# Optimization experiments

Measured on AMD Instinct MI355X. Metric: run time of the kernel, lower is better.

Reference implementation:

```python
import jax, jax.numpy as jnp
import numpy as np

P_DROP = 0.2
NEG_SLOPE = 0.2


def setup_inputs() -> dict:
    key = jax.random.key(0)
    ks = jax.random.split(key, 12)
    N, E = 50000, 800000
    IN, H1, H2, OUT = 256, 256, 128, 64
    x = jax.random.normal(ks[0], (N, IN), dtype=jnp.float32)
    adj_rows = jax.random.randint(ks[1], (E,), 0, N, dtype=jnp.int32)
    adj_cols = jax.random.randint(ks[2], (E,), 0, N, dtype=jnp.int32)
    adj_vals = jax.random.uniform(ks[3], (E,), dtype=jnp.float32)
    W1 = jax.random.normal(ks[4], (H1, IN), dtype=jnp.float32) * (1.0 / np.sqrt(IN))
    b1 = jax.random.normal(ks[5], (H1,), dtype=jnp.float32) * 0.01
    W2 = jax.random.normal(ks[6], (H2, H1), dtype=jnp.float32) * (1.0 / np.sqrt(H1))
    b2 = jax.random.normal(ks[7], (H2,), dtype=jnp.float32) * 0.01
    W3 = jax.random.normal(ks[8], (OUT, H2), dtype=jnp.float32) * (1.0 / np.sqrt(H2))
    b3 = jax.random.normal(ks[9], (OUT,), dtype=jnp.float32) * 0.01
    mask1 = jax.random.bernoulli(ks[10], 1.0 - P_DROP, (N, H1))
    mask2 = jax.random.bernoulli(ks[11], 1.0 - P_DROP, (N, H2))
    return {"x": x, "adj_rows": adj_rows, "adj_cols": adj_cols, "adj_vals": adj_vals,
            "W1": W1, "b1": b1, "W2": W2, "b2": b2, "W3": W3, "b3": b3,
            "mask1": mask1, "mask2": mask2}


def _spmm(rows, cols, vals, h, n_nodes):
    # sparse adjacency matmul: out[r] = sum_e vals[e] * h[cols[e]] for rows[e]==r
    msgs = vals[:, None] * h[cols]  # [E, d] irregular gather
    return jax.ops.segment_sum(msgs, rows, num_segments=n_nodes)


def _gcn_layer(x, W, b, rows, cols, vals, n_nodes):
    h = x @ W.T + b  # nn.Linear
    return _spmm(rows, cols, vals, h, n_nodes)


def reference(x, adj_rows, adj_cols, adj_vals, W1, b1, W2, b2, W3, b3, mask1, mask2):
    N = x.shape[0]
    keep = 1.0 / (1.0 - P_DROP)
    h = _gcn_layer(x, W1, b1, adj_rows, adj_cols, adj_vals, N)
    h = jnp.where(h >= 0, h, NEG_SLOPE * h)
    h = jnp.where(mask1, h * keep, 0.0)
    h = _gcn_layer(h, W2, b2, adj_rows, adj_cols, adj_vals, N)
    h = jnp.where(h >= 0, h, NEG_SLOPE * h)
    h = jnp.where(mask2, h * keep, 0.0)
    z = _gcn_layer(h, W3, b3, adj_rows, adj_cols, adj_vals, N)
    return z
```

## Files before the change

### kernel.cpp

```cpp
#include <hip/hip_runtime.h>


typedef unsigned short ushort_t;
typedef __attribute__((ext_vector_type(8))) short bf16x8;
typedef __attribute__((ext_vector_type(4))) float f32x4;
typedef __attribute__((ext_vector_type(2))) unsigned int u32x2;
typedef __attribute__((ext_vector_type(4))) unsigned int u32x4;

__device__ __forceinline__ float bf2f(ushort_t u) {
  return __uint_as_float(((unsigned int)u) << 16);
}
__device__ __forceinline__ ushort_t f2bf(float f) {
  unsigned int u = __float_as_uint(f);
  return (ushort_t)((u + 0x7FFFu + ((u >> 16) & 1u)) >> 16);
}
__device__ __forceinline__ float read_f(const void* p, int fm, size_t i) {
  return fm ? bf2f(((const ushort_t*)p)[i]) : ((const float*)p)[i];
}

__device__ __forceinline__ size_t frag_off(int m, int k, int K) {
  return (size_t)(m >> 4) * 16 * K + ((size_t)(k >> 5) << 9) +
         (((k >> 3) & 3) << 7) + ((m & 15) << 3) + (k & 7);
}

__global__ void prep_kernel(const void* __restrict__ x,
                            const void* __restrict__ m1,
                            const void* __restrict__ m2,
                            int* __restrict__ modes,
                            int* __restrict__ zero_region, int zn,
                            const void* __restrict__ W1, const void* __restrict__ W2,
                            const void* __restrict__ W3,
                            const void* __restrict__ b1, const void* __restrict__ b2,
                            const void* __restrict__ b3,
                            ushort_t* __restrict__ whi, ushort_t* __restrict__ wlo,
                            float* __restrict__ biasf,
                            int n1, int n2, int n3, int h1, int h2, int h3,
                            int K1, int K2, int K3) {
  if (blockIdx.x == 0) {
    __shared__ int bfok;
    if (threadIdx.x == 0) bfok = 1;
    __syncthreads();
    for (int i = threadIdx.x; i < 8192; i += blockDim.x) {
      ushort_t h = ((const ushort_t*)x)[i];
      int e = (h >> 7) & 0xFF;
      if (!(h == 0 || (e >= 95 && e <= 133))) atomicAnd(&bfok, 0);
    }
    __syncthreads();
    if (threadIdx.x == 0) modes[0] = bfok;
  } else if (blockIdx.x <= 2) {
    const void* p = (blockIdx.x == 1) ? m1 : m2;
    __shared__ int ok[4];
    if (threadIdx.x < 4) ok[threadIdx.x] = 1;
    __syncthreads();
    for (int i = threadIdx.x; i < 4096; i += blockDim.x) {
      unsigned int w = ((const unsigned int*)p)[i];
      if (!(w == 0u || w == 1u)) atomicAnd(&ok[0], 0);
      if (!(w == 0u || w == 0x3F800000u)) atomicAnd(&ok[1], 0);
      unsigned int h16 = w >> 16, l16 = w & 0xFFFFu;
      if (!((h16 == 0u || h16 == 0x3F80u) && (l16 == 0u || l16 == 0x3F80u)))
        atomicAnd(&ok[2], 0);
      if (((w | (w >> 8) | (w >> 16) | (w >> 24)) & 0xFEu) != 0u) atomicAnd(&ok[3], 0);
    }
    __syncthreads();
    if (threadIdx.x == 0)
      modes[blockIdx.x] = ok[0] ? 1 : (ok[1] ? 2 : (ok[2] ? 3 : 0));
  } else if (blockIdx.x < 35) {
    __shared__ int bfok;
    if (threadIdx.x == 0) bfok = 1;
    __syncthreads();
    for (int i = threadIdx.x; i < 8192; i += blockDim.x) {
      ushort_t h = ((const ushort_t*)x)[i];
      int e = (h >> 7) & 0xFF;
      if (!(h == 0 || (e >= 95 && e <= 133))) atomicAnd(&bfok, 0);
    }
    __syncthreads();
    int fm = bfok;
    int wtot = n1 + n2 + n3;
    int total = wtot + h1 + h2 + h3;
    for (int i = (blockIdx.x - 3) * 256 + threadIdx.x; i < total; i += 32 * 256) {
      if (i < wtot) {
        const void* src; int j, K; size_t base;
        if (i < n1) { src = W1; j = i; K = K1; base = 0; }
        else if (i < n1 + n2) { src = W2; j = i - n1; K = K2; base = n1; }
        else { src = W3; j = i - n1 - n2; K = K3; base = (size_t)n1 + n2; }
        int n = j / K, k = j - n * K;
        float v = read_f(src, fm, j);
        ushort_t h = f2bf(v);
        size_t o = base + frag_off(n, k, K);
        whi[o] = h;
        wlo[o] = f2bf(v - bf2f(h));
      } else {
        int k = i - wtot;
        const void* src; int j;
        if (k < h1) { src = b1; j = k; }
        else if (k < h1 + h2) { src = b2; j = k - h1; }
        else { src = b3; j = k - h1 - h2; }
        biasf[k] = read_f(src, fm, j);
      }
    }
  } else {
    int i = (blockIdx.x - 35) * blockDim.x + threadIdx.x;
    int stride = (gridDim.x - 35) * blockDim.x;
    for (; i < zn; i += stride) zero_region[i] = 0;
  }
}

__global__ __launch_bounds__(256) void scan_fused_kernel(
    const int* __restrict__ cnt8, int* __restrict__ pub,
    int* __restrict__ row_start, int n) {
  int b = blockIdx.x, t = threadIdx.x;
  int i = b * 256 + t;
  int v = 0;
  if (i < n) {
#pragma unroll
    for (int x = 0; x < 8; ++x) v += cnt8[(size_t)x * n + i];
  }
  __shared__ int s[256];
  s[t] = v;
  __syncthreads();
  for (int off = 1; off < 256; off <<= 1) {
    int a_ = s[t];
    int y_ = (t >= off) ? s[t - off] : 0;
    __syncthreads();
    s[t] = a_ + y_;
    __syncthreads();
  }
  int incl = s[t];
  int total = s[255];
  if (t == 0)
    __hip_atomic_store(&pub[b], (total << 1) | 1, __ATOMIC_RELEASE,
                       __HIP_MEMORY_SCOPE_AGENT);
  int contrib = 0;
  for (int t0 = t; t0 < b; t0 += 256) {
    int p;
    do {
      p = __hip_atomic_load(&pub[t0], __ATOMIC_ACQUIRE,
                            __HIP_MEMORY_SCOPE_AGENT);
    } while (!(p & 1));
    contrib += (p >> 1);
  }
  __syncthreads();
  s[t] = contrib;
  __syncthreads();
  for (int off = 128; off > 0; off >>= 1) {
    if (t < off) s[t] += s[t + off];
    __syncthreads();
  }
  int base = s[0];
  if (i < n) row_start[i] = base + incl - v;
  if (i == n - 1) row_start[n] = base + incl;
}

__global__ void hist_bin_kernel(
    const int* __restrict__ rows, const int* __restrict__ cols,
    const void* __restrict__ vals, const int* __restrict__ fm_p,
    int* __restrict__ cnt8, int* __restrict__ binfill,
    int2* __restrict__ bins, int cap, int use_bins, int2* __restrict__ ovf,
    int E, int Nrows, const void* __restrict__ x, ushort_t* __restrict__ xbf,
    int K1, int nx) {
  int fm = *fm_p;
  const int BIN_BLOCKS = 1024;
  if (blockIdx.x < BIN_BLOCKS) {
    int xcd = blockIdx.x & 7;
    int* cnt_s = cnt8 + (size_t)xcd * Nrows;
    if (use_bins) {
      __shared__ int hist[8];
      __shared__ int gbase[8];
      __shared__ int pfx[8];
      __shared__ int2 stage[1024];
      int tid = threadIdx.x;
      for (int tb = blockIdx.x; tb * 1024 < E; tb += BIN_BLOCKS) {
        int base = tb * 1024;
        if (tid < 8) hist[tid] = 0;
        __syncthreads();
        int rr[4], cc[4], pp[4], rk[4]; float vv[4];
#pragma unroll
        for (int j = 0; j < 4; ++j) {
          int i = base + j * 256 + tid;
          if (i < E) {
            rr[j] = rows[i]; cc[j] = cols[i]; vv[j] = read_f(vals, fm, i);
            atomicAdd(&cnt_s[rr[j]], 1);
            pp[j] = rr[j] >> 13;
            rk[j] = atomicAdd(&hist[pp[j]], 1);
          } else {
            pp[j] = -1;
          }
        }
        __syncthreads();
        if (tid == 0) {
          int s = 0;
#pragma unroll
          for (int q = 0; q < 8; ++q) { pfx[q] = s; s += hist[q]; }
        }
        if (tid < 8)
          gbase[tid] = atomicAdd(&binfill[(xcd << 4) + tid], hist[tid]);
        __syncthreads();
#pragma unroll
        for (int j = 0; j < 4; ++j) {
          if (pp[j] >= 0)
            stage[pfx[pp[j]] + rk[j]] =
                make_int2((rr[j] << 16) | cc[j], __float_as_int(vv[j]));
        }
        __syncthreads();
        int total = pfx[7] + hist[7];
        for (int k = tid; k < total; k += 256) {
          int p = 0;
#pragma unroll
          for (int q = 1; q < 8; ++q) p += (k >= pfx[q]);
          int2 ent = stage[k];
          int pos = gbase[p] + (k - pfx[p]);
          if (pos < cap) {
            bins[(size_t)((xcd << 3) + p) * cap + pos] = ent;
          } else {
            int op = atomicAdd(&binfill[128], 1);
            ovf[op] = ent;
          }
        }
        __syncthreads();
      }
    } else {
      int i = blockIdx.x * blockDim.x + threadIdx.x;
      int stride = BIN_BLOCKS * blockDim.x;
      for (; i < E; i += stride) atomicAdd(&cnt_s[rows[i]], 1);
    }
  } else {
    if (fm == 1) return;
    int nx4 = nx / 4;
    int i = (blockIdx.x - BIN_BLOCKS) * blockDim.x + threadIdx.x;
    int stride = (gridDim.x - BIN_BLOCKS) * blockDim.x;
    for (; i < nx4; i += stride) {
      int m = i / (K1 / 4);
      int k0 = (i - m * (K1 / 4)) * 4;
      f32x4 v = ((const f32x4*)x)[i];
      ushort_t p0 = f2bf(v[0]), p1 = f2bf(v[1]), p2 = f2bf(v[2]), p3 = f2bf(v[3]);
      size_t o = frag_off(m, k0, K1);
      *(u32x2*)(xbf + o) = (u32x2){
          (unsigned int)p0 | ((unsigned int)p1 << 16),
          (unsigned int)p2 | ((unsigned int)p3 << 16)};
    }
  }
}

template<int KC>
__device__ __forceinline__ void load_afrag(const ushort_t* __restrict__ A,
                                           const ushort_t* __restrict__ Xrow,
                                           bool rowA, int mtile, int K,
                                           int lane, int mr, int quad, int M,
                                           bf16x8* dst) {
  if (rowA) {
    int rr = mtile * 16 + mr;
    if (rr >= M) rr = M - 1;
    const ushort_t* ap = Xrow + (size_t)rr * K + quad * 8;
#pragma unroll
    for (int kc = 0; kc < KC; ++kc) dst[kc] = *(const bf16x8*)(ap + kc * 32);
  } else {
    const ushort_t* ap = A + (size_t)mtile * 16 * K + lane * 8;
#pragma unroll
    for (int kc = 0; kc < KC; ++kc) dst[kc] = *(const bf16x8*)(ap + kc * 512);
  }
}

template<int KC>
__device__ __forceinline__ void gemm_dev(
    int vbid, int nblk, int tid,
    const ushort_t* __restrict__ A, const ushort_t* __restrict__ Xrow, int fm,
    const ushort_t* __restrict__ Whi, const ushort_t* __restrict__ Wlo,
    const float* __restrict__ bias, ushort_t* __restrict__ g, int ldg,
    int M, int nct) {
  const int K = KC * 32;
  int wave = tid >> 6, lane = tid & 63;
  int gw = vbid * 4 + wave;
  int NW = nblk * 4;
  int mr = lane & 15, quad = lane >> 4;
  int ct = gw % nct;
  int nrt = (M + 15) >> 4;
  int ntasks = nct * nrt;
  if (gw >= ntasks) return;

  bool rowA = (Xrow != nullptr) && (fm != 0);

  bf16x8 wh[KC], wl[KC];
  {
    const ushort_t* wp = Whi + (size_t)ct * 16 * K + lane * 8;
    const ushort_t* wq = Wlo + (size_t)ct * 16 * K + lane * 8;
#pragma unroll
    for (int kc = 0; kc < KC; ++kc) {
      wh[kc] = *(const bf16x8*)(wp + kc * 512);
      wl[kc] = *(const bf16x8*)(wq + kc * 512);
    }
  }
  int col = ct * 16 + mr;
  float bv = bias[col];

  int task = gw;
  bf16x8 af[KC];
  load_afrag<KC>(A, Xrow, rowA, task / nct, K, lane, mr, quad, M, af);

#pragma unroll 1
  for (;;) {
    int next = task + NW;
    bool has_next = next < ntasks;
    bf16x8 afn[KC];
    if (has_next)
      load_afrag<KC>(A, Xrow, rowA, next / nct, K, lane, mr, quad, M, afn);

    f32x4 acc[4];
#pragma unroll
    for (int t = 0; t < 4; ++t) acc[t] = (f32x4){0.f, 0.f, 0.f, 0.f};
#pragma unroll
    for (int kc = 0; kc < KC; ++kc) {
      acc[(2 * kc) & 3] = __builtin_amdgcn_mfma_f32_16x16x32_bf16(af[kc], wh[kc], acc[(2 * kc) & 3], 0, 0, 0);
      acc[(2 * kc + 1) & 3] = __builtin_amdgcn_mfma_f32_16x16x32_bf16(af[kc], wl[kc], acc[(2 * kc + 1) & 3], 0, 0, 0);
    }
    int m0 = (task / nct) * 16;
#pragma unroll
    for (int r = 0; r < 4; ++r) {
      int row = m0 + quad * 4 + r;
      float s = ((acc[0][r] + acc[1][r]) + (acc[2][r] + acc[3][r])) + bv;
      if (row < M) g[(size_t)row * ldg + col] = f2bf(s);
    }
    if (!has_next) break;
#pragma unroll
    for (int kc = 0; kc < KC; ++kc) af[kc] = afn[kc];
    task = next;
  }
}

template<int KC>
__global__ __launch_bounds__(256) void gemm_breg_kernel(
    const ushort_t* __restrict__ A,
    const ushort_t* __restrict__ Xrow, const int* __restrict__ fm_p,
    const ushort_t* __restrict__ Whi, const ushort_t* __restrict__ Wlo,
    const float* __restrict__ bias, ushort_t* __restrict__ g, int ldg,
    int M, int nct) {
  gemm_dev<KC>(blockIdx.x, gridDim.x, threadIdx.x, A, Xrow, *fm_p,
               Whi, Wlo, bias, g, ldg, M, nct);
}

__global__ __launch_bounds__(256) void scatter_gemm_kernel(
    const int2* __restrict__ bins, const int* __restrict__ binfill,
    const int* __restrict__ row_start, int* __restrict__ fill,
    int2* __restrict__ ecv, int cap, const int2* __restrict__ ovf,
    const int* __restrict__ rows, const int* __restrict__ cols,
    const void* __restrict__ vals, const int* __restrict__ fm_p,
    int use_bins, int E,
    const ushort_t* __restrict__ A, const ushort_t* __restrict__ Xrow,
    const ushort_t* __restrict__ Whi, const ushort_t* __restrict__ Wlo,
    const float* __restrict__ bias, ushort_t* __restrict__ g, int ldg,
    int M, int nct) {
  if (blockIdx.x >= 1024) {
    gemm_dev<8>(blockIdx.x - 1024, 1024, threadIdx.x, A, Xrow, *fm_p,
                Whi, Wlo, bias, g, ldg, M, nct);
    return;
  }
  if (use_bins) {
    int p = blockIdx.x & 7, q = blockIdx.x >> 3;
#pragma unroll 1
    for (int x = 0; x < 8; ++x) {
      int n = binfill[x * 16 + p];
      if (n > cap) n = cap;
      const int2* bp = bins + (size_t)((x << 3) + p) * cap;
      for (int e = q * 256 + (int)threadIdx.x; e < n; e += 128 * 256) {
        int2 ent = bp[e];
        int r = ((unsigned int)ent.x) >> 16;
        int c = ent.x & 0xFFFF;
        int pos = atomicAdd(&fill[r], 1);
        ecv[row_start[r] + pos] = make_int2(c, ent.y);
      }
    }
    int ovfn = binfill[128];
    for (int e = blockIdx.x * 256 + (int)threadIdx.x; e < ovfn; e += 1024 * 256) {
      int2 ent = ovf[e];
      int r = ((unsigned int)ent.x) >> 16;
      int c = ent.x & 0xFFFF;
      int pos = atomicAdd(&fill[r], 1);
      ecv[row_start[r] + pos] = make_int2(c, ent.y);
    }
  } else {
    int fm = *fm_p;
    for (int i = blockIdx.x * 256 + (int)threadIdx.x; i < E; i += 1024 * 256) {
      int r = rows[i];
      int pos = atomicAdd(&fill[r], 1);
      ecv[row_start[r] + pos] = make_int2(cols[i], __float_as_int(read_f(vals, fm, i)));
    }
  }
}

template<int VEC, int CHUNK, bool CLAMP>
__device__ __forceinline__ void spmm_chunk(const int2* __restrict__ ecv,
                                           int base, int e1,
                                           const ushort_t* __restrict__ G,
                                           int D, int f0, float* a) {
  int2 cv[CHUNK];
#pragma unroll
  for (int j = 0; j < CHUNK; ++j) {
    int ee = base + j;
    if (CLAMP) ee = (ee < e1) ? ee : e1 - 1;
    cv[j] = ecv[ee];
  }
  float v[CHUNK];
#pragma unroll
  for (int j = 0; j < CHUNK; ++j) {
    v[j] = __int_as_float(cv[j].y);
    if (CLAMP && (base + j >= e1)) v[j] = 0.f;
  }
  if (VEC == 4) {
    u32x2 gg[CHUNK];
#pragma unroll
    for (int j = 0; j < CHUNK; ++j)
      gg[j] = *(const u32x2*)(G + (size_t)cv[j].x * D + f0);
#pragma unroll
    for (int j = 0; j < CHUNK; ++j) {
      a[0] += v[j] * bf2f((ushort_t)gg[j][0]);
      a[1] += v[j] * bf2f((ushort_t)(gg[j][0] >> 16));
      a[2] += v[j] * bf2f((ushort_t)gg[j][1]);
      a[3] += v[j] * bf2f((ushort_t)(gg[j][1] >> 16));
    }
  } else if (VEC == 2) {
    unsigned int gg[CHUNK];
#pragma unroll
    for (int j = 0; j < CHUNK; ++j)
      gg[j] = *(const unsigned int*)(G + (size_t)cv[j].x * D + f0);
#pragma unroll
    for (int j = 0; j < CHUNK; ++j) {
      a[0] += v[j] * bf2f((ushort_t)gg[j]);
      a[1] += v[j] * bf2f((ushort_t)(gg[j] >> 16));
    }
  } else {
    ushort_t h[CHUNK];
#pragma unroll
    for (int j = 0; j < CHUNK; ++j) h[j] = G[(size_t)cv[j].x * D + f0];
#pragma unroll
    for (int j = 0; j < CHUNK; ++j) a[0] += v[j] * bf2f(h[j]);
  }
}

template<int MODE, int VEC>
__global__ __launch_bounds__(256) void spmm8_kernel(
    const int* __restrict__ row_start, const int2* __restrict__ ecv,
    const ushort_t* __restrict__ G, int D,
    const void* __restrict__ mask, const int* __restrict__ mmode_p,
    void* __restrict__ outp, int N) {
  __shared__ ushort_t stage[1024];
  int wave = threadIdx.x >> 6, lane = threadIdx.x & 63;
  int r = blockIdx.x * 4 + wave;
  bool active = r < N;
  float a[VEC];
#pragma unroll
  for (int q = 0; q < VEC; ++q) a[q] = 0.f;
  int f0 = lane * VEC;

  bool keep[VEC];
#pragma unroll
  for (int q = 0; q < VEC; ++q) keep[q] = true;
  if (MODE == 1 && active) {
    size_t om = (size_t)r * D + f0;
    int mm = *mmode_p;
    if (mm == 1 || mm == 2) {
      if (VEC == 4) {
        u32x4 mv = *(const u32x4*)((const unsigned int*)mask + om);
#pragma unroll
        for (int q = 0; q < VEC; ++q) keep[q] = mv[q] != 0u;
      } else if (VEC == 2) {
        u32x2 mv = *(const u32x2*)((const unsigned int*)mask + om);
#pragma unroll
        for (int q = 0; q < VEC; ++q) keep[q] = mv[q] != 0u;
      } else {
        keep[0] = ((const unsigned int*)mask)[om] != 0u;
      }
    } else if (mm == 3) {
      if (VEC == 4) {
        u32x2 mv = *(const u32x2*)((const ushort_t*)mask + om);
        keep[0] = (mv[0] & 0xFFFFu) != 0u; keep[1] = (mv[0] >> 16) != 0u;
        keep[2] = (mv[1] & 0xFFFFu) != 0u; keep[3] = (mv[1] >> 16) != 0u;
      } else if (VEC == 2) {
        unsigned int mv = *(const unsigned int*)((const ushort_t*)mask + om);
        keep[0] = (mv & 0xFFFFu) != 0u; keep[1] = (mv >> 16) != 0u;
      } else {
        keep[0] = ((const ushort_t*)mask)[om] != 0;
      }
    } else {
      if (VEC == 4) {
        unsigned int mv = *(const unsigned int*)((const unsigned char*)mask + om);
        keep[0] = (mv & 0xFFu) != 0u;         keep[1] = ((mv >> 8) & 0xFFu) != 0u;
        keep[2] = ((mv >> 16) & 0xFFu) != 0u; keep[3] = (mv >> 24) != 0u;
      } else if (VEC == 2) {
        unsigned int mv = *(const unsigned short*)((const unsigned char*)mask + om);
        keep[0] = (mv & 0xFFu) != 0u; keep[1] = ((mv >> 8) & 0xFFu) != 0u;
      } else {
        keep[0] = ((const unsigned char*)mask)[om] != 0;
      }
    }
  }

  if (active) {
    int e  = __builtin_amdgcn_readfirstlane(row_start[r]);
    int e1 = __builtin_amdgcn_readfirstlane(row_start[r + 1]);
    for (; e + 16 <= e1; e += 16)
      spmm_chunk<VEC, 16, false>(ecv, e, e1, G, D, f0, a);
    for (; e < e1; e += 8)
      spmm_chunk<VEC, 8, true>(ecv, e, e1, G, D, f0, a);
  }

  if (MODE == 1) {
    if (active) {
#pragma unroll
      for (int q = 0; q < VEC; ++q) {
        float t = a[q];
        t = (t >= 0.f) ? t : 0.2f * t;
        t = keep[q] ? t * 1.25f : 0.f;
        stage[wave * D + f0 + q] = f2bf(t);
      }
    }
    __syncthreads();
    if (threadIdx.x < D) {
      int g = threadIdx.x >> 3, s = threadIdx.x & 7;
      int kc = g >> 2, quad = g & 3;
      int sr = s >> 1;
      int r0 = blockIdx.x * 4;
      if (r0 + sr < N) {
        int kk = kc * 32 + quad * 8 + (s & 1) * 4;
        size_t dst = (size_t)(r0 >> 4) * 16 * D + ((size_t)kc << 9) +
                     (quad << 7) + ((r0 & 15) << 3) + s * 4;
        *(u32x2*)((ushort_t*)outp + dst) = *(const u32x2*)(stage + sr * D + kk);
      }
    }
  } else {
    if (active) {
      size_t o = (size_t)r * D + f0;
#pragma unroll
      for (int q = 0; q < VEC; ++q) ((float*)outp)[o + q] = a[q];
    }
  }
}

extern "C" void kernel_launch(void* const* d_in, const int* in_sizes, int n_in,
                              void* d_out, int out_size, void* d_ws, size_t ws_size,
                              hipStream_t stream) {
  const void* x     = d_in[0];
  const int*  rows  = (const int*)d_in[1];
  const int*  cols  = (const int*)d_in[2];
  const void* vals  = d_in[3];
  const void* W1    = d_in[4];
  const void* b1    = d_in[5];
  const void* W2    = d_in[6];
  const void* b2    = d_in[7];
  const void* W3    = d_in[8];
  const void* b3    = d_in[9];
  const void* mask1 = d_in[10];
  const void* mask2 = d_in[11];

  const int H1  = in_sizes[5];
  const int H2  = in_sizes[7];
  const int OUT = in_sizes[9];
  const int IN  = in_sizes[4] / H1;
  const int N   = in_sizes[0] / IN;
  const int E   = in_sizes[1];
  const int W1n = in_sizes[4], W2n = in_sizes[6], W3n = in_sizes[8];
  const int Np  = ((N + 15) / 16) * 16;
  const int CAP = (E >> 5) + 2048;
  const int use_bins = (N <= 65535) ? 1 : 0;
  const int P = (N + 255) / 256;

  char* ws = (char*)d_ws;
  size_t off = 0;
  auto alloc = [&](size_t bytes) -> void* {
    void* p = ws + off;
    off = (off + bytes + 255) & ~(size_t)255;
    return p;
  };
  int*      modes     = (int*)alloc(4 * 4);
  int*      row_start = (int*)alloc((size_t)(N + 1) * 4);
  int*      meta      = (int*)alloc(((size_t)9 * N + 512) * 4);
  int2*     ecv       = (int2*)alloc((size_t)E * 8);
  int2*     bins      = (int2*)alloc((size_t)64 * CAP * 8);
  int2*     ovf       = (int2*)alloc((size_t)E * 8);
  ushort_t* whi       = (ushort_t*)alloc((size_t)(W1n + W2n + W3n) * 2);
  ushort_t* wlo       = (ushort_t*)alloc((size_t)(W1n + W2n + W3n) * 2);
  float*    biasf     = (float*)alloc((size_t)(H1 + H2 + OUT) * 4);
  ushort_t* bufA      = (ushort_t*)alloc((size_t)Np * H1 * 2);
  ushort_t* bufB      = (ushort_t*)alloc((size_t)Np * H1 * 2);
  ushort_t* bufC      = (ushort_t*)alloc((size_t)Np * H1 * 2);

  int* fmode   = modes;
  int* mm1     = modes + 1;
  int* mm2     = modes + 2;
  int* cnt8    = meta;
  int* fill    = meta + 8 * N;
  int* binfill = meta + 9 * N;
  int* pub     = meta + 9 * N + 256;
  ushort_t* w1hi = whi,             *w1lo = wlo;
  ushort_t* w2hi = whi + W1n,       *w2lo = wlo + W1n;
  ushort_t* w3hi = whi + W1n + W2n, *w3lo = wlo + W1n + W2n;

  prep_kernel<<<512, 256, 0, stream>>>(
      x, mask1, mask2, modes, meta, 9 * N + 512,
      W1, W2, W3, b1, b2, b3, whi, wlo, biasf,
      W1n, W2n, W3n, H1, H2, OUT, IN, H1, H2);

  hist_bin_kernel<<<2048, 256, 0, stream>>>(
      rows, cols, vals, fmode, cnt8, binfill, bins, CAP, use_bins, ovf,
      E, N, x, bufA, IN, N * IN);

  scan_fused_kernel<<<P, 256, 0, stream>>>(cnt8, pub, row_start, N);

  scatter_gemm_kernel<<<2048, 256, 0, stream>>>(
      bins, binfill, row_start, fill, ecv, CAP, ovf,
      rows, cols, vals, fmode, use_bins, E,
      bufA, (const ushort_t*)x, w1hi, w1lo, biasf, bufB, H1, N, H1 / 16);

  int spmm_grid = (N + 3) / 4;
  const int GEMM_BLOCKS = 1024;

  spmm8_kernel<1, 4><<<spmm_grid, 256, 0, stream>>>(
      row_start, ecv, bufB, H1, mask1, mm1, bufC, N);
  gemm_breg_kernel<8><<<GEMM_BLOCKS, 256, 0, stream>>>(
      bufC, nullptr, fmode, w2hi, w2lo, biasf + H1, bufB, H2, N, H2 / 16);
  spmm8_kernel<1, 2><<<spmm_grid, 256, 0, stream>>>(
      row_start, ecv, bufB, H2, mask2, mm2, bufA, N);
  gemm_breg_kernel<4><<<GEMM_BLOCKS, 256, 0, stream>>>(
      bufA, nullptr, fmode, w3hi, w3lo, biasf + H1 + H2, bufB, OUT, N, OUT / 16);
  spmm8_kernel<0, 1><<<spmm_grid, 256, 0, stream>>>(
      row_start, ecv, bufB, OUT, nullptr, fmode, d_out, N);
}
```

Measured before the change: 428.4 us.

## Replace global row-count atomics with per-bin shared-memory histograms and offsets

Moves per-row edge counting out of the binning pass, where it used global atomics, into a new count kernel that builds an 8192-row shared-memory histogram per (xcd, partition) bin. The scan now also emits per-bin start offsets, so the scatter pass can assign CSR slots with shared-memory atomics instead of global fill atomics. Overflow edges carry a precomputed rank so they are placed without atomics. Scatter blocks drop from 1024 to 64, which lowers scatter parallelism, and bufC now aliases the bins buffer to save memory.

```diff
diff --git a/kernel.cpp b/kernel.cpp
--- a/kernel.cpp
+++ b/kernel.cpp
@@ -105,64 +105,17 @@
   }
 }
 
-__global__ __launch_bounds__(256) void scan_fused_kernel(
-    const int* __restrict__ cnt8, int* __restrict__ pub,
-    int* __restrict__ row_start, int n) {
-  int b = blockIdx.x, t = threadIdx.x;
-  int i = b * 256 + t;
-  int v = 0;
-  if (i < n) {
-#pragma unroll
-    for (int x = 0; x < 8; ++x) v += cnt8[(size_t)x * n + i];
-  }
-  __shared__ int s[256];
-  s[t] = v;
-  __syncthreads();
-  for (int off = 1; off < 256; off <<= 1) {
-    int a_ = s[t];
-    int y_ = (t >= off) ? s[t - off] : 0;
-    __syncthreads();
-    s[t] = a_ + y_;
-    __syncthreads();
-  }
-  int incl = s[t];
-  int total = s[255];
-  if (t == 0)
-    __hip_atomic_store(&pub[b], (total << 1) | 1, __ATOMIC_RELEASE,
-                       __HIP_MEMORY_SCOPE_AGENT);
-  int contrib = 0;
-  for (int t0 = t; t0 < b; t0 += 256) {
-    int p;
-    do {
-      p = __hip_atomic_load(&pub[t0], __ATOMIC_ACQUIRE,
-                            __HIP_MEMORY_SCOPE_AGENT);
-    } while (!(p & 1));
-    contrib += (p >> 1);
-  }
-  __syncthreads();
-  s[t] = contrib;
-  __syncthreads();
-  for (int off = 128; off > 0; off >>= 1) {
-    if (t < off) s[t] += s[t + off];
-    __syncthreads();
-  }
-  int base = s[0];
-  if (i < n) row_start[i] = base + incl - v;
-  if (i == n - 1) row_start[n] = base + incl;
-}
-
 __global__ void hist_bin_kernel(
     const int* __restrict__ rows, const int* __restrict__ cols,
     const void* __restrict__ vals, const int* __restrict__ fm_p,
-    int* __restrict__ cnt8, int* __restrict__ binfill,
-    int2* __restrict__ bins, int cap, int use_bins, int2* __restrict__ ovf,
+    int* __restrict__ h8, int* __restrict__ cnt_ovf, int* __restrict__ binfill,
+    int2* __restrict__ bins, int cap, int use_bins, int4* __restrict__ ovf,
     int E, int Nrows, const void* __restrict__ x, ushort_t* __restrict__ xbf,
     int K1, int nx) {
   int fm = *fm_p;
   const int BIN_BLOCKS = 1024;
   if (blockIdx.x < BIN_BLOCKS) {
     int xcd = blockIdx.x & 7;
-    int* cnt_s = cnt8 + (size_t)xcd * Nrows;
     if (use_bins) {
       __shared__ int hist[8];
       __shared__ int gbase[8];
@@ -179,7 +132,6 @@
           int i = base + j * 256 + tid;
           if (i < E) {
             rr[j] = rows[i]; cc[j] = cols[i]; vv[j] = read_f(vals, fm, i);
-            atomicAdd(&cnt_s[rr[j]], 1);
             pp[j] = rr[j] >> 13;
             rk[j] = atomicAdd(&hist[pp[j]], 1);
           } else {
@@ -212,13 +164,16 @@
           if (pos < cap) {
             bins[(size_t)((xcd << 3) + p) * cap + pos] = ent;
           } else {
+            int r = ((unsigned int)ent.x) >> 16;
+            int orank = atomicAdd(&cnt_ovf[r], 1);
             int op = atomicAdd(&binfill[128], 1);
-            ovf[op] = ent;
+            ovf[op] = make_int4(r, ent.x & 0xFFFF, ent.y, orank);
           }
         }
         __syncthreads();
       }
     } else {
+      int* cnt_s = h8 + (size_t)xcd * Nrows;
       int i = blockIdx.x * blockDim.x + threadIdx.x;
       int stride = BIN_BLOCKS * blockDim.x;
       for (; i < E; i += stride) atomicAdd(&cnt_s[rows[i]], 1);
@@ -239,6 +194,89 @@
           (unsigned int)p2 | ((unsigned int)p3 << 16)};
     }
   }
+}
+
+__global__ __launch_bounds__(256) void count_kernel(
+    const int2* __restrict__ bins, const int* __restrict__ binfill,
+    int cap, int* __restrict__ h8, int Nrows, int use_bins) {
+  if (!use_bins) return;
+  int x = blockIdx.x >> 3, p = blockIdx.x & 7;
+  __shared__ int hist[8192];
+  for (int i = threadIdx.x; i < 8192; i += 256) hist[i] = 0;
+  __syncthreads();
+  int n = binfill[x * 16 + p];
+  if (n > cap) n = cap;
+  const int2* bp = bins + (size_t)((x << 3) + p) * cap;
+  for (int e = threadIdx.x; e < n; e += 256) {
+    int r = ((unsigned int)bp[e].x) >> 16;
+    atomicAdd(&hist[r & 8191], 1);
+  }
+  __syncthreads();
+  int r0 = p << 13;
+  for (int i = threadIdx.x; i < 8192; i += 256) {
+    int r = r0 + i;
+    if (r < Nrows) h8[(size_t)x * Nrows + r] = hist[i];
+  }
+}
+
+__global__ __launch_bounds__(256) void scan_fused_kernel(
+    const int* __restrict__ h8, const int* __restrict__ cnt_ovf,
+    int* __restrict__ pub, int* __restrict__ row_start,
+    int* __restrict__ sb8, int n) {
+  int b = blockIdx.x, t = threadIdx.x;
+  int i = b * 256 + t;
+  int hx[8];
+  int v = 0, ov = 0;
+  if (i < n) {
+#pragma unroll
+    for (int x = 0; x < 8; ++x) { hx[x] = h8[(size_t)x * n + i]; v += hx[x]; }
+    ov = cnt_ovf[i];
+  } else {
+#pragma unroll
+    for (int x = 0; x < 8; ++x) hx[x] = 0;
+  }
+  int vt = v + ov;
+  __shared__ int s[256];
+  s[t] = vt;
+  __syncthreads();
+  for (int off = 1; off < 256; off <<= 1) {
+    int a_ = s[t];
+    int y_ = (t >= off) ? s[t - off] : 0;
+    __syncthreads();
+    s[t] = a_ + y_;
+    __syncthreads();
+  }
+  int incl = s[t];
+  int total = s[255];
+  if (t == 0)
+    __hip_atomic_store(&pub[b], (total << 1) | 1, __ATOMIC_RELEASE,
+                       __HIP_MEMORY_SCOPE_AGENT);
+  int contrib = 0;
+  for (int t0 = t; t0 < b; t0 += 256) {
+    int p;
+    do {
+      p = __hip_atomic_load(&pub[t0], __ATOMIC_ACQUIRE,
+                            __HIP_MEMORY_SCOPE_AGENT);
+    } while (!(p & 1));
+    contrib += (p >> 1);
+  }
+  __syncthreads();
+  s[t] = contrib;
+  __syncthreads();
+  for (int off = 128; off > 0; off >>= 1) {
+    if (t < off) s[t] += s[t + off];
+    __syncthreads();
+  }
+  int base = s[0];
+  int rs = base + incl - vt;
+  if (i < n) {
+    row_start[i] = rs;
+    int acc = rs;
+#pragma unroll
+    for (int x = 0; x < 8; ++x) { sb8[(size_t)x * n + i] = acc; acc += hx[x]; }
+    sb8[(size_t)8 * n + i] = acc;
+  }
+  if (i == n - 1) row_start[n] = base + incl;
 }
 
 template<int KC>
@@ -340,7 +378,8 @@
 __global__ __launch_bounds__(256) void scatter_gemm_kernel(
     const int2* __restrict__ bins, const int* __restrict__ binfill,
     const int* __restrict__ row_start, int* __restrict__ fill,
-    int2* __restrict__ ecv, int cap, const int2* __restrict__ ovf,
+    const int* __restrict__ sb8, int Nrows,
+    int2* __restrict__ ecv, int cap, const int4* __restrict__ ovf,
     const int* __restrict__ rows, const int* __restrict__ cols,
     const void* __restrict__ vals, const int* __restrict__ fm_p,
     int use_bins, int E,
@@ -348,37 +387,37 @@
     const ushort_t* __restrict__ Whi, const ushort_t* __restrict__ Wlo,
     const float* __restrict__ bias, ushort_t* __restrict__ g, int ldg,
     int M, int nct) {
-  if (blockIdx.x >= 1024) {
-    gemm_dev<8>(blockIdx.x - 1024, 1024, threadIdx.x, A, Xrow, *fm_p,
+  __shared__ int sbl[8192];
+  if (blockIdx.x >= 64) {
+    gemm_dev<8>(blockIdx.x - 64, 1024, threadIdx.x, A, Xrow, *fm_p,
                 Whi, Wlo, bias, g, ldg, M, nct);
     return;
   }
   if (use_bins) {
-    int p = blockIdx.x & 7, q = blockIdx.x >> 3;
-#pragma unroll 1
-    for (int x = 0; x < 8; ++x) {
-      int n = binfill[x * 16 + p];
-      if (n > cap) n = cap;
-      const int2* bp = bins + (size_t)((x << 3) + p) * cap;
-      for (int e = q * 256 + (int)threadIdx.x; e < n; e += 128 * 256) {
-        int2 ent = bp[e];
-        int r = ((unsigned int)ent.x) >> 16;
-        int c = ent.x & 0xFFFF;
-        int pos = atomicAdd(&fill[r], 1);
-        ecv[row_start[r] + pos] = make_int2(c, ent.y);
-      }
+    int x = blockIdx.x >> 3, p = blockIdx.x & 7;
+    int r0 = p << 13;
+    for (int i = threadIdx.x; i < 8192; i += 256) {
+      int r = r0 + i;
+      sbl[i] = (r < Nrows) ? sb8[(size_t)x * Nrows + r] : 0;
+    }
+    __syncthreads();
+    int n = binfill[x * 16 + p];
+    if (n > cap) n = cap;
+    const int2* bp = bins + (size_t)((x << 3) + p) * cap;
+    for (int e = threadIdx.x; e < n; e += 256) {
+      int2 ent = bp[e];
+      int r = ((unsigned int)ent.x) >> 16;
+      int pos = atomicAdd(&sbl[r & 8191], 1);
+      ecv[pos] = make_int2(ent.x & 0xFFFF, ent.y);
     }
     int ovfn = binfill[128];
-    for (int e = blockIdx.x * 256 + (int)threadIdx.x; e < ovfn; e += 1024 * 256) {
-      int2 ent = ovf[e];
-      int r = ((unsigned int)ent.x) >> 16;
-      int c = ent.x & 0xFFFF;
-      int pos = atomicAdd(&fill[r], 1);
-      ecv[row_start[r] + pos] = make_int2(c, ent.y);
+    for (int e = blockIdx.x * 256 + (int)threadIdx.x; e < ovfn; e += 64 * 256) {
+      int4 t = ovf[e];
+      ecv[sb8[(size_t)8 * Nrows + t.x] + t.w] = make_int2(t.y, t.z);
     }
   } else {
     int fm = *fm_p;
-    for (int i = blockIdx.x * 256 + (int)threadIdx.x; i < E; i += 1024 * 256) {
+    for (int i = blockIdx.x * 256 + (int)threadIdx.x; i < E; i += 64 * 256) {
       int r = rows[i];
       int pos = atomicAdd(&fill[r], 1);
       ecv[row_start[r] + pos] = make_int2(cols[i], __float_as_int(read_f(vals, fm, i)));
@@ -571,41 +610,45 @@
   };
   int*      modes     = (int*)alloc(4 * 4);
   int*      row_start = (int*)alloc((size_t)(N + 1) * 4);
-  int*      meta      = (int*)alloc(((size_t)9 * N + 512) * 4);
+  int*      meta      = (int*)alloc(((size_t)10 * N + 512) * 4);
+  int*      sb8       = (int*)alloc((size_t)9 * N * 4);
   int2*     ecv       = (int2*)alloc((size_t)E * 8);
   int2*     bins      = (int2*)alloc((size_t)64 * CAP * 8);
-  int2*     ovf       = (int2*)alloc((size_t)E * 8);
+  int4*     ovf       = (int4*)alloc((size_t)E * 16);
   ushort_t* whi       = (ushort_t*)alloc((size_t)(W1n + W2n + W3n) * 2);
   ushort_t* wlo       = (ushort_t*)alloc((size_t)(W1n + W2n + W3n) * 2);
   float*    biasf     = (float*)alloc((size_t)(H1 + H2 + OUT) * 4);
   ushort_t* bufA      = (ushort_t*)alloc((size_t)Np * H1 * 2);
   ushort_t* bufB      = (ushort_t*)alloc((size_t)Np * H1 * 2);
-  ushort_t* bufC      = (ushort_t*)alloc((size_t)Np * H1 * 2);
+  ushort_t* bufC      = (ushort_t*)bins;
 
   int* fmode   = modes;
   int* mm1     = modes + 1;
   int* mm2     = modes + 2;
-  int* cnt8    = meta;
-  int* fill    = meta + 8 * N;
-  int* binfill = meta + 9 * N;
-  int* pub     = meta + 9 * N + 256;
+  int* h8      = meta;
+  int* cnt_ovf = meta + 8 * N;
+  int* fill    = meta + 9 * N;
+  int* binfill = meta + 10 * N;
+  int* pub     = meta + 10 * N + 256;
   ushort_t* w1hi = whi,             *w1lo = wlo;
   ushort_t* w2hi = whi + W1n,       *w2lo = wlo + W1n;
   ushort_t* w3hi = whi + W1n + W2n, *w3lo = wlo + W1n + W2n;
 
   prep_kernel<<<512, 256, 0, stream>>>(
-      x, mask1, mask2, modes, meta, 9 * N + 512,
+      x, mask1, mask2, modes, meta, 10 * N + 512,
       W1, W2, W3, b1, b2, b3, whi, wlo, biasf,
       W1n, W2n, W3n, H1, H2, OUT, IN, H1, H2);
 
   hist_bin_kernel<<<2048, 256, 0, stream>>>(
-      rows, cols, vals, fmode, cnt8, binfill, bins, CAP, use_bins, ovf,
+      rows, cols, vals, fmode, h8, cnt_ovf, binfill, bins, CAP, use_bins, ovf,
       E, N, x, bufA, IN, N * IN);
 
-  scan_fused_kernel<<<P, 256, 0, stream>>>(cnt8, pub, row_start, N);
-
-  scatter_gemm_kernel<<<2048, 256, 0, stream>>>(
-      bins, binfill, row_start, fill, ecv, CAP, ovf,
+  count_kernel<<<64, 256, 0, stream>>>(bins, binfill, CAP, h8, N, use_bins);
+
+  scan_fused_kernel<<<P, 256, 0, stream>>>(h8, cnt_ovf, pub, row_start, sb8, N);
+
+  scatter_gemm_kernel<<<1088, 256, 0, stream>>>(
+      bins, binfill, row_start, fill, sb8, N, ecv, CAP, ovf,
       rows, cols, vals, fmode, use_bins, E,
       bufA, (const ushort_t*)x, w1hi, w1lo, biasf, bufB, H1, N, H1 / 16);
 
```

Result: faster. 406.7 us (median of 2 runs) (-5.1%).
